# Kernel tuning notes

Hardware: AMD Instinct MI355X
Metric: run time of the kernel (lower is better)

Reference implementation:

```python
import jax, jax.numpy as jnp
import numpy as np

STRIDE = (1, 2, 2)
PADDING = ((2, 2), (3, 3), (3, 3))


def setup_inputs() -> dict:
    key = jax.random.key(0)
    kx, kw, kb = jax.random.split(key, 3)
    x = jax.random.normal(kx, (8, 3, 16, 112, 112), dtype=jnp.float32)
    weight = jax.random.normal(kw, (64, 3, 5, 7, 7), dtype=jnp.float32)
    bias = jax.random.normal(kb, (64,), dtype=jnp.float32)
    return {"x": x, "weight": weight, "bias": bias}


def reference(x, weight, bias):
    # NCDHW input, OIDHW weight -> NCDHW output; same math as the
    # torch module's explicit slice-multiply-sum conv3d.
    out = jax.lax.conv_general_dilated(
        x, weight,
        window_strides=STRIDE,
        padding=PADDING,
        dimension_numbers=("NCDHW", "OIDHW", "NCDHW"),
    )
    out = out + bias[None, :, None, None, None]
    return out
```

## Files before the change

### kernel.cpp

```cpp
#include <hip/hip_runtime.h>


typedef __attribute__((ext_vector_type(8)))  short short8;
typedef __attribute__((ext_vector_type(4)))  float f32x4;
typedef __attribute__((ext_vector_type(16))) float f32x16;

#define CI 3
#define DI 16
#define HI 112
#define WI 112
#define CO 64
#define DO_ 16
#define HO 56
#define WO 56
#define HW_IN 12544
#define DHWO 50176

#define NROW 105
#define NCH 27

#define XP_ROW 144
#define XP_H   119
#define XP_D   20
#define XPAD_BYTES  (8*3*XP_D*XP_H*XP_ROW*2)
#define WBUF_OFF    XPAD_BYTES
#define WS_NEED     (WBUF_OFF + NCH*4*64*16 + 4096)

#define SEG_SH 1296
#define SEG_DW 648

__device__ __forceinline__ unsigned short f2bf(float f) {
    unsigned u = __float_as_uint(f);
    return (unsigned short)((u + 0x7FFFu + ((u >> 16) & 1u)) >> 16);
}
__device__ __forceinline__ unsigned pk_bf16(float a, float b) {
    unsigned r;
    asm("v_cvt_pk_bf16_f32 %0, %1, %2" : "=v"(r) : "v"(a), "v"(b));
    return r;
}

__device__ __forceinline__ constexpr int rb2(int r) {
    const int rc = (r > 104) ? 104 : r;
    const int c  = rc / 35;
    const int kd = (rc / 7) % 5;
    const int kh = rc % 7;
    return (c * 6 + kd) * SEG_DW + kh * (XP_ROW / 2);
}

#define XP_THREADS (8*3*XP_D*XP_H*18)
#define XP_BLOCKS  4017

__global__ void prep_all(const float* __restrict__ x, const float* __restrict__ wgt,
                         unsigned* __restrict__ xp, short8* __restrict__ wbuf) {
    if (blockIdx.x < XP_BLOCKS) {
        const int g = blockIdx.x * 256 + threadIdx.x;
        if (g >= XP_THREADS) return;
        const int s8 = g % 18;
        int r = g / 18;
        const int hp = r % XP_H; r /= XP_H;
        const int dp = r % XP_D; r /= XP_D;
        const int c  = r % 3;
        const int n  = r / 3;
        const int din = dp - 2, hin = hp - 3;
        const bool rowok = ((unsigned)din < (unsigned)DI) && ((unsigned)hin < (unsigned)HI);
        float v[8];
        const int w0 = 8 * s8 - 3;
        if (rowok && s8 >= 1 && s8 <= 13) {
            const float* xr = x + ((n * CI + c) * DI + din) * HW_IN + hin * WI + w0;
            #pragma unroll
            for (int j = 0; j < 8; ++j) v[j] = xr[j];
        } else if (rowok && (s8 == 0 || s8 == 14)) {
            const float* xr = x + ((n * CI + c) * DI + din) * HW_IN + hin * WI;
            #pragma unroll
            for (int j = 0; j < 8; ++j) {
                const int w = w0 + j;
                v[j] = ((unsigned)w < (unsigned)WI) ? xr[w] : 0.0f;
            }
        } else {
            #pragma unroll
            for (int j = 0; j < 8; ++j) v[j] = 0.0f;
        }
        uint4 o;
        o.x = pk_bf16(v[0], v[1]); o.y = pk_bf16(v[2], v[3]);
        o.z = pk_bf16(v[4], v[5]); o.w = pk_bf16(v[6], v[7]);
        *reinterpret_cast<uint4*>(xp + 4 * (size_t)g) = o;
    } else {
        const int t = (blockIdx.x - XP_BLOCKS) * 256 + threadIdx.x;
        const int lane = t & 63;
        const int cf   = t >> 6;
        const int q    = cf & 3;
        const int a    = q & 1;
        const int ks   = q >> 1;
        const int ch   = cf >> 2;
        const int l31  = lane & 31;
        const int hl   = lane >> 5;
        const int co   = a * 32 + l31;
        const int r    = ch * 4 + ks * 2 + hl;
        const int rc   = (r > 104) ? 104 : r;
        const int c    = rc / 35;
        const int kd   = (rc / 7) % 5;
        const int kh   = rc % 7;
        const float* wsrc = wgt + (((co * CI + c) * 5 + kd) * 7 + kh) * 7;
        short8 v;
        #pragma unroll
        for (int j = 0; j < 8; ++j) {
            float w = (r < NROW && j < 7) ? wsrc[j] : 0.0f;
            v[j] = (short)f2bf(w);
        }
        wbuf[(size_t)cf * 64 + lane] = v;
    }
}

#define MFMA32(A, B, C) __builtin_amdgcn_mfma_f32_32x32x16_bf16(A, B, C, 0, 0, 0)

__launch_bounds__(256, 3)
__global__ void conv3d_v11(const unsigned short* __restrict__ xpad,
                           const short8* __restrict__ wbuf,
                           const float* __restrict__ bias,
                           float* __restrict__ out) {
    __shared__ __align__(16) unsigned short xl[18 * SEG_SH];

    const int tid = threadIdx.x;
    int b = ((blockIdx.x & 7) * 224) + (blockIdx.x >> 3);
    const int ht  = b % 28;  b /= 28;
    const int ddp = b & 7;
    const int n   = b >> 3;
    const int ho0 = ht * 2;
    const int dd0 = ddp * 2;

    const int lane = tid & 63;
    const int wid  = tid >> 6;

    {
        const size_t nb = (size_t)(n * CI) * XP_D;
        for (int s = wid; s < 18; s += 4) {
            const int c = s / 6;
            const int p = s - c * 6;
            const char* gsrc = (const char*)(xpad +
                ((nb + (size_t)c * XP_D + (dd0 + p)) * XP_H + 2 * ho0) * XP_ROW)
                + lane * 16;
            char* ldst = (char*)&xl[s * SEG_SH];
            __builtin_amdgcn_global_load_lds(
                (const __attribute__((address_space(1))) void*)(gsrc),
                (__attribute__((address_space(3))) void*)(ldst), 16, 0, 0);
            __builtin_amdgcn_global_load_lds(
                (const __attribute__((address_space(1))) void*)(gsrc + 1024),
                (__attribute__((address_space(3))) void*)(ldst + 1024), 16, 0, 0);
            if (lane < 34)
                __builtin_amdgcn_global_load_lds(
                    (const __attribute__((address_space(1))) void*)(gsrc + 2048),
                    (__attribute__((address_space(3))) void*)(ldst + 2048), 16, 0, 0);
        }
    }

    const int ddl = wid & 1;
    const int hoL = wid >> 1;
    const int l31 = lane & 31;
    const int hl  = lane >> 5;
    const int tspB = ddl * SEG_DW + hoL * 144 + l31;

    f32x16 acc[2][2];
    #pragma unroll
    for (int a = 0; a < 2; ++a) {
        f32x16 bv;
        #pragma unroll
        for (int g = 0; g < 16; ++g)
            bv[g] = bias[a * 32 + (g & 3) + 8 * (g >> 2) + 4 * hl];
        acc[a][0] = bv; acc[a][1] = bv;
    }

    const short8* wbp = wbuf + lane;
    const unsigned* xlu = reinterpret_cast<const unsigned*>(xl);

    union BxU { unsigned u[4]; short8 s; };
    short8 As[3][4];
    BxU    Bs[2][4];

    auto loadA = [&](int ch, int slot) {
        const int nq = (ch == NCH - 1) ? 2 : 4;
        #pragma unroll
        for (int q = 0; q < 4; ++q)
            if (q < nq) As[slot][q] = wbp[(ch * 4 + q) * 64];
    };
    auto loadB = [&](int ch, int slot) {
        const int nks = (ch == NCH - 1) ? 1 : 2;
        #pragma unroll
        for (int ks = 0; ks < 2; ++ks) {
            if (ks < nks) {
                const int r0 = ch * 4 + ks * 2;
                const int b0 = rb2(r0);
                const int b1 = rb2(r0 + 1);
                const int base = b0 + hl * (b1 - b0);
                const unsigned* xp = xlu + base + tspB;
                #pragma unroll
                for (int f = 0; f < 2; ++f) {
                    const unsigned* p = xp + f * 32;
                    Bs[slot][ks * 2 + f].u[0] = p[0];
                    Bs[slot][ks * 2 + f].u[1] = p[1];
                    Bs[slot][ks * 2 + f].u[2] = p[2];
                    Bs[slot][ks * 2 + f].u[3] = p[3];
                }
            }
        }
    };

    loadA(0, 0);
    loadA(1, 1);
    __syncthreads();
    loadB(0, 0);

    #pragma unroll
    for (int ch = 0; ch < NCH; ++ch) {
        if (ch + 2 < NCH) loadA(ch + 2, (ch + 2) % 3);
        if (ch + 1 < NCH) loadB(ch + 1, (ch + 1) & 1);
        __builtin_amdgcn_sched_barrier(0);
        __builtin_amdgcn_s_setprio(1);
        const int sA = ch % 3;
        const int sB = ch & 1;
        #pragma unroll
        for (int a = 0; a < 2; ++a) {
            #pragma unroll
            for (int f = 0; f < 2; ++f) {
                acc[a][f] = MFMA32(As[sA][0 + a], Bs[sB][0 + f].s, acc[a][f]);
                if (ch != NCH - 1)
                    acc[a][f] = MFMA32(As[sA][2 + a], Bs[sB][2 + f].s, acc[a][f]);
            }
        }
        __builtin_amdgcn_s_setprio(0);
        __builtin_amdgcn_sched_barrier(0);
    }

    const int dd = dd0 + ddl;
    const int ho = ho0 + hoL;
    const size_t obase = (size_t)n * CO * DHWO + (size_t)dd * 3136 + ho * WO;
    #pragma unroll
    for (int f = 0; f < 2; ++f) {
        const int wo = f * 32 + l31;
        if (f == 0 || l31 < 24) {
            #pragma unroll
            for (int a = 0; a < 2; ++a) {
                #pragma unroll
                for (int g = 0; g < 16; ++g) {
                    const int co = a * 32 + (g & 3) + 8 * (g >> 2) + 4 * hl;
                    out[obase + (size_t)co * DHWO + wo] = acc[a][f][g];
                }
            }
        }
    }
}

#define FB_LR 13
#define FB_LROWS 234
#define FB_LWS 144
#define FB_XLSZ (FB_LROWS*FB_LWS)
#define MFMA16(A, B, C) __builtin_amdgcn_mfma_f32_16x16x32_bf16(A, B, C, 0, 0, 0)

__global__ void prep_weights_fb(const float* __restrict__ wgt, short8* __restrict__ wbuf) {
    const int t    = blockIdx.x * 64 + threadIdx.x;
    const int lane = t & 63;
    const int cf   = t >> 6;
    const int l15  = lane & 15;
    const int kgrp = lane >> 4;
    const int co   = (cf & 3) * 16 + l15;
    const int rr   = (cf >> 2) * 4 + kgrp;
    const int rc   = (rr < NROW) ? rr : (NROW - 1);
    const int c    = rc / 35;
    const int kd   = (rc / 7) % 5;
    const int kh   = rc % 7;
    const float* wsrc = wgt + (((co * CI + c) * 5 + kd) * 7 + kh) * 7;
    short8 v;
    #pragma unroll
    for (int j = 0; j < 8; ++j) {
        float w = (rr < NROW && j < 7) ? wsrc[j] : 0.0f;
        v[j] = (short)f2bf(w);
    }
    wbuf[(size_t)cf * 64 + lane] = v;
}

__launch_bounds__(512, 2)
__global__ void conv3d_mfma4(const float* __restrict__ x,
                             const short8* __restrict__ wbuf,
                             const float* __restrict__ bias,
                             float* __restrict__ out) {
    __shared__ unsigned short xl[FB_XLSZ];
    __shared__ int rowg[FB_LROWS];
    __shared__ unsigned short tabr[108];

    const int tid = threadIdx.x;
    int b = blockIdx.x;
    const int ht  = b % 14;  b /= 14;
    const int ddp = b % 8;
    const int n   = b / 8;
    const int ho0 = ht * 4;
    const int dd0 = ddp * 2;

    if (tid < FB_LROWS) {
        const int c   = tid / (6 * FB_LR);
        const int rem = tid - c * (6 * FB_LR);
        const int p   = rem / FB_LR;
        const int rl  = rem - p * FB_LR;
        const int din = dd0 - 2 + p;
        const int hin = 2 * ho0 - 3 + rl;
        const bool ok = ((unsigned)din < (unsigned)DI) && ((unsigned)hin < (unsigned)HI);
        rowg[tid] = ok ? ((n * CI + c) * DI + din) * HW_IN + hin * WI : -1;
    }
    if (tid < 108) {
        const int rc = (tid < NROW) ? tid : (NROW - 1);
        const int c  = rc / 35;
        const int kd = (rc / 7) % 5;
        const int kh = rc % 7;
        tabr[tid] = (unsigned short)(((c * 6 + kd) * FB_LR + kh) * FB_LWS);
    }
    __syncthreads();

    const int lane = tid & 63;
    const int wid  = tid >> 6;

    for (int row = wid; row < FB_LROWS; row += 8) {
        const int base = rowg[row];
        unsigned short* dst = &xl[row * FB_LWS];
        if (lane < 57) {
            float v0 = 0.0f, v1 = 0.0f;
            const int w0 = 2 * lane - 1;
            if (base >= 0) {
                if (lane >= 1)  v0 = x[base + w0];
                if (lane <= 55) v1 = x[base + w0 + 1];
            }
            *reinterpret_cast<unsigned*>(&dst[2 * lane + 2]) = pk_bf16(v0, v1);
        } else {
            const int dw = (lane == 57) ? 0 : lane;
            *reinterpret_cast<unsigned*>(&dst[2 * dw]) = 0u;
        }
    }
    __syncthreads();

    const int ddl  = wid & 1;
    const int hoL  = wid >> 1;
    const int l15  = lane & 15;
    const int kgrp = lane >> 4;
    const int woff = ddl * (FB_LR * FB_LWS) + hoL * (2 * FB_LWS);

    f32x4 acc[4][4];
    #pragma unroll
    for (int a = 0; a < 4; ++a) {
        f32x4 bv;
        #pragma unroll
        for (int r = 0; r < 4; ++r) bv[r] = bias[a * 16 + kgrp * 4 + r];
        #pragma unroll
        for (int f = 0; f < 4; ++f) acc[a][f] = bv;
    }

    const short8* wbp = wbuf + lane;
    short8 Acur[4], Anxt[4];
    #pragma unroll
    for (int a = 0; a < 4; ++a) Acur[a] = wbp[a * 64];
    int tb = (int)tabr[kgrp] + woff;

    const unsigned* xlu = reinterpret_cast<const unsigned*>(xl);

    for (int ch = 0; ch < NCH; ++ch) {
        int tbn = 0;
        if (ch + 1 < NCH) {
            tbn = (int)tabr[(ch + 1) * 4 + kgrp] + woff;
            #pragma unroll
            for (int a = 0; a < 4; ++a) Anxt[a] = wbp[((ch + 1) * 4 + a) * 64];
        }
        const unsigned* xp = xlu + (tb >> 1) + l15;
        union { unsigned u[4]; short8 s; } bx[4];
        #pragma unroll
        for (int f = 0; f < 4; ++f) {
            const unsigned* p = xp + f * 16;
            bx[f].u[0] = p[0]; bx[f].u[1] = p[1];
            bx[f].u[2] = p[2]; bx[f].u[3] = p[3];
        }
        #pragma unroll
        for (int f = 0; f < 4; ++f) {
            acc[0][f] = MFMA16(Acur[0], bx[f].s, acc[0][f]);
            acc[1][f] = MFMA16(Acur[1], bx[f].s, acc[1][f]);
            acc[2][f] = MFMA16(Acur[2], bx[f].s, acc[2][f]);
            acc[3][f] = MFMA16(Acur[3], bx[f].s, acc[3][f]);
        }
        tb = tbn;
        #pragma unroll
        for (int a = 0; a < 4; ++a) Acur[a] = Anxt[a];
    }

    const int dd = dd0 + ddl;
    const int ho = ho0 + hoL;
    #pragma unroll
    for (int f = 0; f < 4; ++f) {
        const int wo = f * 16 + l15;
        if (f < 3 || l15 < 8) {
            float* op = out + (((size_t)(n * CO) * DO_ + dd) * HO + ho) * WO + wo;
            #pragma unroll
            for (int a = 0; a < 4; ++a) {
                const int co = a * 16 + kgrp * 4;
                #pragma unroll
                for (int r = 0; r < 4; ++r)
                    op[(size_t)(co + r) * DHWO] = acc[a][f][r];
            }
        }
    }
}

extern "C" void kernel_launch(void* const* d_in, const int* in_sizes, int n_in,
                              void* d_out, int out_size, void* d_ws, size_t ws_size,
                              hipStream_t stream) {
    const float* x    = (const float*)d_in[0];
    const float* wgt  = (const float*)d_in[1];
    const float* bias = (const float*)d_in[2];
    float* out        = (float*)d_out;

    if (ws_size >= (size_t)WS_NEED) {
        unsigned* xpad = (unsigned*)d_ws;
        short8* wbuf   = (short8*)((char*)d_ws + WBUF_OFF);
        hipLaunchKernelGGL(prep_all, dim3(XP_BLOCKS + 27, 1, 1), dim3(256, 1, 1), 0,
                           stream, x, wgt, xpad, wbuf);
        hipLaunchKernelGGL(conv3d_v11, dim3(1792, 1, 1), dim3(256, 1, 1), 0, stream,
                           (const unsigned short*)xpad, wbuf, bias, out);
    } else {
        short8* wbuf = (short8*)d_ws;
        hipLaunchKernelGGL(prep_weights_fb, dim3(NCH * 4, 1, 1), dim3(64, 1, 1), 0,
                           stream, wgt, wbuf);
        hipLaunchKernelGGL(conv3d_mfma4, dim3(896, 1, 1), dim3(512, 1, 1), 0, stream,
                           x, wbuf, bias, out);
    }
}
```

Before: 71.78 us.

## Shrink padded row stride and drop register double-buffering to raise occupancy

The padded bf16 input row shrinks from 144 to 120 elements, which cuts the preprocessing pass and the per-block LDS footprint (with a small slack region). The main conv kernel now asks for 4 blocks per SIMD instead of 3. To fit that, the B-operand register prefetch and the triple-buffered A prefetch become a single B buffer loaded in-iteration plus a double-buffered A, and the sched_barriers are removed. More concurrent waves should hide latency, but each wave loses explicit software pipelining of LDS reads ahead of the MFMAs, and the tighter 120-element stride must still cover every window the kernel reads.

```diff
diff --git a/kernel.cpp b/kernel.cpp
--- a/kernel.cpp
+++ b/kernel.cpp
@@ -19,15 +19,16 @@
 #define NROW 105
 #define NCH 27
 
-#define XP_ROW 144
+#define XP_ROW 120
 #define XP_H   119
 #define XP_D   20
 #define XPAD_BYTES  (8*3*XP_D*XP_H*XP_ROW*2)
 #define WBUF_OFF    XPAD_BYTES
 #define WS_NEED     (WBUF_OFF + NCH*4*64*16 + 4096)
 
-#define SEG_SH 1296
-#define SEG_DW 648
+#define SEG_SH 1080
+#define SEG_DW 540
+#define ROW_DW 60
 
 __device__ __forceinline__ unsigned short f2bf(float f) {
     unsigned u = __float_as_uint(f);
@@ -44,19 +45,19 @@
     const int c  = rc / 35;
     const int kd = (rc / 7) % 5;
     const int kh = rc % 7;
-    return (c * 6 + kd) * SEG_DW + kh * (XP_ROW / 2);
-}
-
-#define XP_THREADS (8*3*XP_D*XP_H*18)
-#define XP_BLOCKS  4017
+    return (c * 6 + kd) * SEG_DW + kh * ROW_DW;
+}
+
+#define XP_THREADS (8*3*XP_D*XP_H*15)
+#define XP_BLOCKS  3347
 
 __global__ void prep_all(const float* __restrict__ x, const float* __restrict__ wgt,
                          unsigned* __restrict__ xp, short8* __restrict__ wbuf) {
     if (blockIdx.x < XP_BLOCKS) {
         const int g = blockIdx.x * 256 + threadIdx.x;
         if (g >= XP_THREADS) return;
-        const int s8 = g % 18;
-        int r = g / 18;
+        const int s8 = g % 15;
+        int r = g / 15;
         const int hp = r % XP_H; r /= XP_H;
         const int dp = r % XP_D; r /= XP_D;
         const int c  = r % 3;
@@ -113,12 +114,12 @@
 
 #define MFMA32(A, B, C) __builtin_amdgcn_mfma_f32_32x32x16_bf16(A, B, C, 0, 0, 0)
 
-__launch_bounds__(256, 3)
-__global__ void conv3d_v11(const unsigned short* __restrict__ xpad,
+__launch_bounds__(256, 4)
+__global__ void conv3d_v13(const unsigned short* __restrict__ xpad,
                            const short8* __restrict__ wbuf,
                            const float* __restrict__ bias,
                            float* __restrict__ out) {
-    __shared__ __align__(16) unsigned short xl[18 * SEG_SH];
+    __shared__ __align__(16) unsigned short xl[18 * SEG_SH + 128];
 
     const int tid = threadIdx.x;
     int b = ((blockIdx.x & 7) * 224) + (blockIdx.x >> 3);
@@ -146,7 +147,7 @@
             __builtin_amdgcn_global_load_lds(
                 (const __attribute__((address_space(1))) void*)(gsrc + 1024),
                 (__attribute__((address_space(3))) void*)(ldst + 1024), 16, 0, 0);
-            if (lane < 34)
+            if (lane < 7)
                 __builtin_amdgcn_global_load_lds(
                     (const __attribute__((address_space(1))) void*)(gsrc + 2048),
                     (__attribute__((address_space(3))) void*)(ldst + 2048), 16, 0, 0);
@@ -157,7 +158,7 @@
     const int hoL = wid >> 1;
     const int l31 = lane & 31;
     const int hl  = lane >> 5;
-    const int tspB = ddl * SEG_DW + hoL * 144 + l31;
+    const int tspB = ddl * SEG_DW + hoL * (2 * ROW_DW) + l31;
 
     f32x16 acc[2][2];
     #pragma unroll
@@ -173,8 +174,8 @@
     const unsigned* xlu = reinterpret_cast<const unsigned*>(xl);
 
     union BxU { unsigned u[4]; short8 s; };
-    short8 As[3][4];
-    BxU    Bs[2][4];
+    short8 As[2][4];
+    BxU    Bs[4];
 
     auto loadA = [&](int ch, int slot) {
         const int nq = (ch == NCH - 1) ? 2 : 4;
@@ -182,7 +183,7 @@
         for (int q = 0; q < 4; ++q)
             if (q < nq) As[slot][q] = wbp[(ch * 4 + q) * 64];
     };
-    auto loadB = [&](int ch, int slot) {
+    auto loadB = [&](int ch) {
         const int nks = (ch == NCH - 1) ? 1 : 2;
         #pragma unroll
         for (int ks = 0; ks < 2; ++ks) {
@@ -195,39 +196,34 @@
                 #pragma unroll
                 for (int f = 0; f < 2; ++f) {
                     const unsigned* p = xp + f * 32;
-                    Bs[slot][ks * 2 + f].u[0] = p[0];
-                    Bs[slot][ks * 2 + f].u[1] = p[1];
-                    Bs[slot][ks * 2 + f].u[2] = p[2];
-                    Bs[slot][ks * 2 + f].u[3] = p[3];
+                    Bs[ks * 2 + f].u[0] = p[0];
+                    Bs[ks * 2 + f].u[1] = p[1];
+                    Bs[ks * 2 + f].u[2] = p[2];
+                    Bs[ks * 2 + f].u[3] = p[3];
                 }
             }
         }
     };
 
     loadA(0, 0);
-    loadA(1, 1);
     __syncthreads();
-    loadB(0, 0);
 
     #pragma unroll
     for (int ch = 0; ch < NCH; ++ch) {
-        if (ch + 2 < NCH) loadA(ch + 2, (ch + 2) % 3);
-        if (ch + 1 < NCH) loadB(ch + 1, (ch + 1) & 1);
-        __builtin_amdgcn_sched_barrier(0);
+        loadB(ch);
+        if (ch + 1 < NCH) loadA(ch + 1, (ch + 1) & 1);
         __builtin_amdgcn_s_setprio(1);
-        const int sA = ch % 3;
-        const int sB = ch & 1;
+        const int s = ch & 1;
         #pragma unroll
         for (int a = 0; a < 2; ++a) {
             #pragma unroll
             for (int f = 0; f < 2; ++f) {
-                acc[a][f] = MFMA32(As[sA][0 + a], Bs[sB][0 + f].s, acc[a][f]);
+                acc[a][f] = MFMA32(As[s][0 + a], Bs[0 + f].s, acc[a][f]);
                 if (ch != NCH - 1)
-                    acc[a][f] = MFMA32(As[sA][2 + a], Bs[sB][2 + f].s, acc[a][f]);
+                    acc[a][f] = MFMA32(As[s][2 + a], Bs[2 + f].s, acc[a][f]);
             }
         }
         __builtin_amdgcn_s_setprio(0);
-        __builtin_amdgcn_sched_barrier(0);
     }
 
     const int dd = dd0 + ddl;
@@ -416,7 +412,7 @@
         short8* wbuf   = (short8*)((char*)d_ws + WBUF_OFF);
         hipLaunchKernelGGL(prep_all, dim3(XP_BLOCKS + 27, 1, 1), dim3(256, 1, 1), 0,
                            stream, x, wgt, xpad, wbuf);
-        hipLaunchKernelGGL(conv3d_v11, dim3(1792, 1, 1), dim3(256, 1, 1), 0, stream,
+        hipLaunchKernelGGL(conv3d_v13, dim3(1792, 1, 1), dim3(256, 1, 1), 0, stream,
                            (const unsigned short*)xpad, wbuf, bias, out);
     } else {
         short8* wbuf = (short8*)d_ws;
```

After: 67.69 us. 1.06x faster.
